# Performance work log

Hardware: AMD Instinct MI355X
Metric: run time of the kernel (lower is better)

## Reference

```python
import jax, jax.numpy as jnp
import numpy as np

B, T, F_IN, H = 64, 256, 2048, 1024


def setup_inputs() -> dict:
    key = jax.random.key(0)
    ks = jax.random.split(key, 8)
    s = 1.0 / np.sqrt(H)
    return {
        "input_var": jax.random.normal(ks[0], (B, T, F_IN), dtype=jnp.float32),
        "input_lengths": jax.random.randint(ks[1], (B,), 1, T + 1, dtype=jnp.int32),
        "W_p": jax.random.uniform(ks[2], (H, F_IN), jnp.float32, -s, s),
        "b_p": jax.random.uniform(ks[3], (H,), jnp.float32, -s, s),
        "w_ih": jax.random.uniform(ks[4], (3 * H, H), jnp.float32, -s, s),
        "w_hh": jax.random.uniform(ks[5], (3 * H, H), jnp.float32, -s, s),
        "b_ih": jax.random.uniform(ks[6], (3 * H,), jnp.float32, -s, s),
        "b_hh": jax.random.uniform(ks[7], (3 * H,), jnp.float32, -s, s),
    }


def reference(input_var, input_lengths, W_p, b_p, w_ih, w_hh, b_ih, b_hh):
    # project video features: (B,T,F) -> (B,T,H)
    emb = jnp.einsum("btf,hf->bth", input_var, W_p) + b_p
    # precompute input-gate contributions for all timesteps: (B,T,3H)
    gx = jnp.einsum("bth,gh->btg", emb, w_ih) + b_ih
    gx_t = jnp.swapaxes(gx, 0, 1)  # time-major (T,B,3H)
    t_idx = jnp.arange(T)
    mask_t = (t_idx[:, None] < input_lengths[None, :])  # (T,B)

    def step(h, inp):
        gi, m = inp  # gi: (B,3H), m: (B,)
        gh = h @ w_hh.T + b_hh  # (B,3H)
        r = jax.nn.sigmoid(gi[:, :H] + gh[:, :H])
        z = jax.nn.sigmoid(gi[:, H:2 * H] + gh[:, H:2 * H])
        n = jnp.tanh(gi[:, 2 * H:] + r * gh[:, 2 * H:])
        h_new = (1.0 - z) * n + z * h
        m2 = m[:, None]
        h = jnp.where(m2, h_new, h)           # packed: hidden frozen past length
        y = jnp.where(m2, h_new, 0.0)         # pad_packed: zeros past length
        return h, y

    h0 = jnp.zeros((B, H), dtype=input_var.dtype)
    _, ys = jax.lax.scan(step, h0, (gx_t, mask_t))  # ys: (T,B,H)
    output = jnp.swapaxes(ys, 0, 1)  # (B,T,H)
    hidden = output[:, -1, :]
    return (output, hidden)
```

## Files before the change

kernel.cpp:

```cpp
#include <hip/hip_runtime.h>
#include <stdint.h>


typedef __bf16 bfx8 __attribute__((ext_vector_type(8)));
typedef float  f32x4 __attribute__((ext_vector_type(4)));
typedef unsigned u32x4 __attribute__((ext_vector_type(4)));
typedef unsigned long long ull;

__global__ void cvt_bf16(const float* __restrict__ in, __bf16* __restrict__ out, int n8) {
    for (int i = blockIdx.x * blockDim.x + threadIdx.x; i < n8; i += gridDim.x * blockDim.x) {
        float4 a = ((const float4*)in)[2 * i];
        float4 b = ((const float4*)in)[2 * i + 1];
        union { __bf16 h[8]; uint4 v; } u;
        u.h[0] = (__bf16)a.x; u.h[1] = (__bf16)a.y; u.h[2] = (__bf16)a.z; u.h[3] = (__bf16)a.w;
        u.h[4] = (__bf16)b.x; u.h[5] = (__bf16)b.y; u.h[6] = (__bf16)b.z; u.h[7] = (__bf16)b.w;
        ((uint4*)out)[i] = u.v;
    }
}

__device__ __forceinline__ void g2l16(const void* g, void* l) {
    __builtin_amdgcn_global_load_lds(
        (__attribute__((address_space(1))) void*)g,
        (__attribute__((address_space(3))) void*)l,
        16, 0, 0);
}


__device__ __forceinline__ void stage_half16(const char* mat, int row0, size_t Kb, int tk,
                                             char* ldsHalf, int sr, int scb, int wave) {
    const char* s0 = mat + (size_t)(row0 + sr) * Kb + ((size_t)tk << 7) + scb;
    g2l16(s0, ldsHalf + (wave << 10));
    g2l16(s0 + (Kb << 6), ldsHalf + 8192 + (wave << 10));
}

#define MFMA16 __builtin_amdgcn_mfma_f32_16x16x32_bf16

template <bool OUTBF16>
__global__ __launch_bounds__(512)
void gemm256(const __bf16* __restrict__ A, const __bf16* __restrict__ W,
             const float* __restrict__ bias, void* __restrict__ C,
             int M, int N, int K)
{
    __shared__ char smem[131072];
    const int tid  = threadIdx.x;
    const int wave = tid >> 6, lane = tid & 63;
    const int q = lane >> 4, r15 = lane & 15;
    const int wm = wave >> 2, wn = wave & 3;

    const int nbx = N >> 8;
    const int nwg = (M >> 8) * nbx;
    const int cpx = nwg >> 3;
    const int wg  = (blockIdx.x & 7) * cpx + (blockIdx.x >> 3);
    const int m0  = (wg / nbx) << 8, n0 = (wg % nbx) << 8;
    const size_t Kb = (size_t)K << 1;
    const int NT = K >> 6;

    const int sr  = tid >> 3;
    const int scb = ((tid ^ (tid >> 3)) & 7) << 4;
    const int sx  = r15 & 7;
    const int la0 = r15 * 128 + ((q ^ sx) << 4);
    const int la1 = r15 * 128 + (((q | 4) ^ sx) << 4);

    const char* Ac = (const char*)A;
    const char* Wc = (const char*)W;

#pragma unroll
    for (int t = 0; t < 2; ++t) {
        char* ab = smem + (t << 15);
        char* bb = smem + 65536 + (t << 15);
        stage_half16(Ac, m0,       Kb, t, ab,         sr, scb, wave);
        stage_half16(Ac, m0 + 128, Kb, t, ab + 16384, sr, scb, wave);
        stage_half16(Wc, n0,       Kb, t, bb,         sr, scb, wave);
        stage_half16(Wc, n0 + 128, Kb, t, bb + 16384, sr, scb, wave);
    }
    asm volatile("s_waitcnt vmcnt(8)" ::: "memory");
    __builtin_amdgcn_s_barrier();

    f32x4 acc[8][4] = {};

    for (int t = 0; t < NT; ++t) {
        const int bsel = t & 1;
        const char* Ab = smem + (bsel << 15) + (wm << 14);
        const char* Bb = smem + 65536 + (bsel << 15) + ((wn >> 1) << 14) + ((wn & 1) << 13);
        const int t2 = t + 2;
        const bool st = t2 < NT;

        bfx8 aw[4][2], b01[2][2], b23[2][2];

#pragma unroll
        for (int m = 0; m < 4; ++m) {
            aw[m][0] = *(const bfx8*)(Ab + (m << 11) + la0);
            aw[m][1] = *(const bfx8*)(Ab + (m << 11) + la1);
        }
#pragma unroll
        for (int n = 0; n < 2; ++n) {
            b01[n][0] = *(const bfx8*)(Bb + (n << 11) + la0);
            b01[n][1] = *(const bfx8*)(Bb + (n << 11) + la1);
        }
        __builtin_amdgcn_s_barrier();
        asm volatile("s_waitcnt lgkmcnt(0)" ::: "memory");
        __builtin_amdgcn_s_setprio(1);
#pragma unroll
        for (int m = 0; m < 4; ++m)
#pragma unroll
            for (int n = 0; n < 2; ++n) {
                acc[m][n] = MFMA16(aw[m][0], b01[n][0], acc[m][n], 0, 0, 0);
                acc[m][n] = MFMA16(aw[m][1], b01[n][1], acc[m][n], 0, 0, 0);
            }
        __builtin_amdgcn_s_setprio(0);
        __builtin_amdgcn_s_barrier();

#pragma unroll
        for (int n = 0; n < 2; ++n) {
            b23[n][0] = *(const bfx8*)(Bb + ((n + 2) << 11) + la0);
            b23[n][1] = *(const bfx8*)(Bb + ((n + 2) << 11) + la1);
        }
        if (st) {
            char* bb = smem + 65536 + (bsel << 15);
            stage_half16(Wc, n0,       Kb, t2, bb,         sr, scb, wave);
            stage_half16(Wc, n0 + 128, Kb, t2, bb + 16384, sr, scb, wave);
        }
        __builtin_amdgcn_s_barrier();
        asm volatile("s_waitcnt lgkmcnt(0)" ::: "memory");
        __builtin_amdgcn_s_setprio(1);
#pragma unroll
        for (int m = 0; m < 4; ++m)
#pragma unroll
            for (int n = 0; n < 2; ++n) {
                acc[m][n + 2] = MFMA16(aw[m][0], b23[n][0], acc[m][n + 2], 0, 0, 0);
                acc[m][n + 2] = MFMA16(aw[m][1], b23[n][1], acc[m][n + 2], 0, 0, 0);
            }
        __builtin_amdgcn_s_setprio(0);
        __builtin_amdgcn_s_barrier();

#pragma unroll
        for (int m = 0; m < 4; ++m) {
            aw[m][0] = *(const bfx8*)(Ab + 8192 + (m << 11) + la0);
            aw[m][1] = *(const bfx8*)(Ab + 8192 + (m << 11) + la1);
        }
        if (st) {
            char* ab = smem + (bsel << 15);
            stage_half16(Ac, m0,       Kb, t2, ab,         sr, scb, wave);
            stage_half16(Ac, m0 + 128, Kb, t2, ab + 16384, sr, scb, wave);
        }
        __builtin_amdgcn_s_barrier();
        asm volatile("s_waitcnt lgkmcnt(0)" ::: "memory");
        __builtin_amdgcn_s_setprio(1);
#pragma unroll
        for (int m = 0; m < 4; ++m)
#pragma unroll
            for (int n = 0; n < 2; ++n) {
                acc[m + 4][n + 2] = MFMA16(aw[m][0], b23[n][0], acc[m + 4][n + 2], 0, 0, 0);
                acc[m + 4][n + 2] = MFMA16(aw[m][1], b23[n][1], acc[m + 4][n + 2], 0, 0, 0);
            }
        __builtin_amdgcn_s_setprio(0);
        __builtin_amdgcn_s_barrier();

        if (t < NT - 2) asm volatile("s_waitcnt vmcnt(8)" ::: "memory");
        else            asm volatile("s_waitcnt vmcnt(0)" ::: "memory");
        __builtin_amdgcn_s_barrier();
        __builtin_amdgcn_s_setprio(1);
#pragma unroll
        for (int m = 0; m < 4; ++m)
#pragma unroll
            for (int n = 0; n < 2; ++n) {
                acc[m + 4][n] = MFMA16(aw[m][0], b01[n][0], acc[m + 4][n], 0, 0, 0);
                acc[m + 4][n] = MFMA16(aw[m][1], b01[n][1], acc[m + 4][n], 0, 0, 0);
            }
        __builtin_amdgcn_s_setprio(0);
        __builtin_amdgcn_s_barrier();
    }

#pragma unroll
    for (int nf = 0; nf < 4; ++nf) {
        const int col = n0 + (wn << 6) + (nf << 4) + r15;
        const float bv = bias[col];
#pragma unroll
        for (int mf = 0; mf < 8; ++mf) {
#pragma unroll
            for (int i = 0; i < 4; ++i) {
                const int row = m0 + (wm << 7) + (mf << 4) + (q << 2) + i;
                const float v = acc[mf][nf][i] + bv;
                if (OUTBF16) ((__bf16*)C)[(size_t)row * N + col] = (__bf16)v;
                else         ((float*)C)[(size_t)row * N + col]  = v;
            }
        }
    }
}

__device__ __forceinline__ float sigm(float x) { return 1.f / (1.f + __expf(-x)); }
__device__ __forceinline__ float tanh_f(float x) { float e = __expf(2.f * x); return 1.f - 2.f / (e + 1.f); }

#define RP 1032

__global__ __launch_bounds__(256, 1)
void rnn_kernel(const float* __restrict__ gx, const int* __restrict__ lens,
                const __bf16* __restrict__ whhb, const float* __restrict__ b_hh,
                char* __restrict__ hbuf,
                float* __restrict__ out,
                unsigned* __restrict__ flags)
{
    __shared__ __bf16 hs[16 * RP];
    __shared__ float  ghs2[3 * 4 * 256];

    const int tid  = threadIdx.x;
    const int wave = tid >> 6, lane = tid & 63;
    const int q = lane >> 4, r15 = lane & 15;
    const int bb = (blockIdx.x & 7) >> 1;
    const int bj = ((blockIdx.x >> 3) << 1) | (blockIdx.x & 1);

    bfx8 Bf[3][8];
#pragma unroll
    for (int g = 0; g < 3; ++g)
#pragma unroll
        for (int kk = 0; kk < 8; ++kk)
            Bf[g][kk] = *(const bfx8*)(whhb
                + ((size_t)((g << 10) + (bj << 4) + r15) << 10)
                + (wave << 8) + (kk << 5) + (q << 3));

    const int m_ = tid >> 4, jj_ = tid & 15;
    const int bglob = (bb << 4) + m_;
    const int jglob = (bj << 4) + jj_;
    const float bhr = b_hh[jglob], bhz = b_hh[1024 + jglob], bhn = b_hh[2048 + jglob];
    const int mylen = lens[bglob];
    const int pd   = (tid & 127) >> 1;
    const int pblk = ((pd >> 1) << 3) | (bb << 1) | (pd & 1);
    const unsigned* fpoll = &flags[pblk << 4];

    const float* gp = gx + (size_t)bglob * 256 * 3072 + jglob;
    float gir = gp[0], giz = gp[1024], gin = gp[2048];
    float hstate = 0.f;

    for (int t = 0; t < 256; ++t) {
        if (t > 0) {
            unsigned tgt = (unsigned)t;
            while (__hip_atomic_load(fpoll, __ATOMIC_RELAXED, __HIP_MEMORY_SCOPE_AGENT) < tgt)
                __builtin_amdgcn_s_sleep(1);
            asm volatile("" ::: "memory");
        }
        {
            const char* sb = hbuf + ((t & 1) << 17) + (bb << 15) + (tid << 4);
            u32x4 r0, r1, r2, r3, r4, r5, r6, r7;
            asm volatile(
                "global_load_dwordx4 %0, %8, off sc1\n\t"
                "global_load_dwordx4 %1, %9, off sc1\n\t"
                "global_load_dwordx4 %2, %10, off sc1\n\t"
                "global_load_dwordx4 %3, %11, off sc1\n\t"
                "global_load_dwordx4 %4, %12, off sc1\n\t"
                "global_load_dwordx4 %5, %13, off sc1\n\t"
                "global_load_dwordx4 %6, %14, off sc1\n\t"
                "global_load_dwordx4 %7, %15, off sc1\n\t"
                "s_waitcnt vmcnt(0)"
                : "=&v"(r0), "=&v"(r1), "=&v"(r2), "=&v"(r3),
                  "=&v"(r4), "=&v"(r5), "=&v"(r6), "=&v"(r7)
                : "v"(sb),          "v"(sb + 4096),  "v"(sb + 8192),  "v"(sb + 12288),
                  "v"(sb + 16384),  "v"(sb + 20480), "v"(sb + 24576), "v"(sb + 28672)
                : "memory");
            const int colb = (tid & 127) << 4;
            const int mh = tid >> 7;
            char* hsb = (char*)hs;
            *(u32x4*)(hsb + (2 * 0 + mh) * 2064 + colb) = r0;
            *(u32x4*)(hsb + (2 * 1 + mh) * 2064 + colb) = r1;
            *(u32x4*)(hsb + (2 * 2 + mh) * 2064 + colb) = r2;
            *(u32x4*)(hsb + (2 * 3 + mh) * 2064 + colb) = r3;
            *(u32x4*)(hsb + (2 * 4 + mh) * 2064 + colb) = r4;
            *(u32x4*)(hsb + (2 * 5 + mh) * 2064 + colb) = r5;
            *(u32x4*)(hsb + (2 * 6 + mh) * 2064 + colb) = r6;
            *(u32x4*)(hsb + (2 * 7 + mh) * 2064 + colb) = r7;
        }
        __syncthreads();

        {
            f32x4 a0 = {0.f, 0.f, 0.f, 0.f}, a1 = a0, a2 = a0;
            const __bf16* hrow = &hs[r15 * RP + (wave << 8)];
#pragma unroll
            for (int kk = 0; kk < 8; ++kk) {
                bfx8 a = *(const bfx8*)(hrow + (kk << 5) + (q << 3));
                a0 = __builtin_amdgcn_mfma_f32_16x16x32_bf16(a, Bf[0][kk], a0, 0, 0, 0);
                a1 = __builtin_amdgcn_mfma_f32_16x16x32_bf16(a, Bf[1][kk], a1, 0, 0, 0);
                a2 = __builtin_amdgcn_mfma_f32_16x16x32_bf16(a, Bf[2][kk], a2, 0, 0, 0);
            }
#pragma unroll
            for (int i2 = 0; i2 < 4; ++i2) {
                int di = (((q << 2) + i2) << 4) + r15;
                ghs2[(wave << 8) + di]        = a0[i2];
                ghs2[1024 + (wave << 8) + di] = a1[i2];
                ghs2[2048 + (wave << 8) + di] = a2[i2];
            }
        }
        __syncthreads();

        float ghr = ghs2[tid] + ghs2[256 + tid] + ghs2[512 + tid] + ghs2[768 + tid] + bhr;
        float ghz = ghs2[1024 + tid] + ghs2[1280 + tid] + ghs2[1536 + tid] + ghs2[1792 + tid] + bhz;
        float ghn = ghs2[2048 + tid] + ghs2[2304 + tid] + ghs2[2560 + tid] + ghs2[2816 + tid] + bhn;
        float rg = sigm(gir + ghr);
        float zg = sigm(giz + ghz);
        float ng = tanh_f(gin + rg * ghn);
        float hnew = (1.f - zg) * ng + zg * hstate;
        bool mk = t < mylen;
        hstate = mk ? hnew : hstate;
        float y = mk ? hnew : 0.f;

        if (t < 255) {
            union { unsigned short us; __bf16 h; } cv; cv.h = (__bf16)hstate;
            unsigned hb = cv.us;
            unsigned nb = (unsigned)__shfl_xor((int)hb, 1);
            if (!(tid & 1)) {
                unsigned dv = hb | (nb << 16);
                unsigned* hw = (unsigned*)(hbuf + (((t + 1) & 1) << 17)
                             + (bglob << 11) + ((bj << 4) + jj_) * 2);
                __hip_atomic_store(hw, dv, __ATOMIC_RELAXED, __HIP_MEMORY_SCOPE_AGENT);
            }
            __syncthreads();
            if (tid == 0)
                __hip_atomic_store(&flags[blockIdx.x << 4], (unsigned)(t + 1),
                                   __ATOMIC_RELAXED, __HIP_MEMORY_SCOPE_AGENT);
            out[(size_t)(bglob * 256 + t) * 1024 + jglob] = y;
            gp += 3072;
            gir = gp[0]; giz = gp[1024]; gin = gp[2048];
        } else {
            out[(size_t)(bglob * 256 + t) * 1024 + jglob] = y;
            out[(size_t)(64 * 256) * 1024 + ((size_t)bglob << 10) + jglob] = y;
        }
    }
}

extern "C" void kernel_launch(void* const* d_in, const int* in_sizes, int n_in,
                              void* d_out, int out_size, void* d_ws, size_t ws_size,
                              hipStream_t stream) {
    const float* input = (const float*)d_in[0];
    const int*   lens  = (const int*)d_in[1];
    const float* W_p   = (const float*)d_in[2];
    const float* b_p   = (const float*)d_in[3];
    const float* w_ih  = (const float*)d_in[4];
    const float* w_hh  = (const float*)d_in[5];
    const float* b_ih  = (const float*)d_in[6];
    const float* b_hh  = (const float*)d_in[7];
    float* out = (float*)d_out;
    char* ws = (char*)d_ws;

    __bf16* Xb   = (__bf16*)(ws + 0);
    __bf16* Wpb  = (__bf16*)(ws + 67108864);
    __bf16* wihb = (__bf16*)(ws + 71303168);
    __bf16* whhb = (__bf16*)(ws + 77594624);
    __bf16* embb = (__bf16*)(ws + 83886080);
    float*  gx   = (float*) (ws + 117440512);
    char* hbuf   = ws + 318767104;
    unsigned* flags = (unsigned*)(ws + 319029248);

    hipMemsetAsync(ws + 318767104, 0, 262144 + 16384, stream);

    cvt_bf16<<<4096, 256, 0, stream>>>(input, Xb, 33554432 / 8);
    cvt_bf16<<<1024, 256, 0, stream>>>(W_p,  Wpb, 2097152 / 8);
    cvt_bf16<<<1536, 256, 0, stream>>>(w_ih, wihb, 3145728 / 8);
    cvt_bf16<<<1536, 256, 0, stream>>>(w_hh, whhb, 3145728 / 8);

    gemm256<true><<<dim3(256), 512, 0, stream>>>(Xb, Wpb, b_p, embb, 16384, 1024, 2048);
    gemm256<false><<<dim3(768), 512, 0, stream>>>(embb, wihb, b_ih, gx, 16384, 3072, 1024);

    rnn_kernel<<<256, 256, 0, stream>>>(gx, lens, whhb, b_hh, hbuf, out, flags);
}
```

Measured before the change: 978.4 us.

## Fuse input-gate projection into recurrent kernel, removing the gx GEMM

Drops the separate emb×w_ih GEMM and its large fp32 gx intermediate. Each RNN block now keeps its w_ih slice in registers and computes the input-gate contributions for step t+1 with MFMA while waiting on step t. The bf16 embedding rows are double-buffered through LDS and prefetched two steps ahead. This removes a full GEMM launch and the gx write/read traffic, but adds register pressure (a second 48-fragment weight set), extra LDS, and more MFMA work inside the latency-critical serial loop.

```diff
diff --git a/kernel.cpp b/kernel.cpp
--- a/kernel.cpp
+++ b/kernel.cpp
@@ -25,6 +25,7 @@
         16, 0, 0);
 }
 
+#define MFMA16 __builtin_amdgcn_mfma_f32_16x16x32_bf16
 
 __device__ __forceinline__ void stage_half16(const char* mat, int row0, size_t Kb, int tk,
                                              char* ldsHalf, int sr, int scb, int wave) {
@@ -32,8 +33,6 @@
     g2l16(s0, ldsHalf + (wave << 10));
     g2l16(s0 + (Kb << 6), ldsHalf + 8192 + (wave << 10));
 }
-
-#define MFMA16 __builtin_amdgcn_mfma_f32_16x16x32_bf16
 
 template <bool OUTBF16>
 __global__ __launch_bounds__(512)
@@ -194,14 +193,16 @@
 #define RP 1032
 
 __global__ __launch_bounds__(256, 1)
-void rnn_kernel(const float* __restrict__ gx, const int* __restrict__ lens,
-                const __bf16* __restrict__ whhb, const float* __restrict__ b_hh,
+void rnn_kernel(const __bf16* __restrict__ emb, const int* __restrict__ lens,
+                const __bf16* __restrict__ whhb, const __bf16* __restrict__ wihb,
+                const float* __restrict__ b_hh, const float* __restrict__ b_ih,
                 char* __restrict__ hbuf,
                 float* __restrict__ out,
                 unsigned* __restrict__ flags)
 {
     __shared__ __bf16 hs[16 * RP];
-    __shared__ float  ghs2[3 * 4 * 256];
+    __shared__ __bf16 ebs[2][16 * RP];
+    __shared__ float  ghs2[4 * 1024];
 
     const int tid  = threadIdx.x;
     const int wave = tid >> 6, lane = tid & 63;
@@ -209,29 +210,73 @@
     const int bb = (blockIdx.x & 7) >> 1;
     const int bj = ((blockIdx.x >> 3) << 1) | (blockIdx.x & 1);
 
-    bfx8 Bf[3][8];
+    bfx8 Bf[3][8], Wf[3][8];
 #pragma unroll
     for (int g = 0; g < 3; ++g)
 #pragma unroll
-        for (int kk = 0; kk < 8; ++kk)
-            Bf[g][kk] = *(const bfx8*)(whhb
-                + ((size_t)((g << 10) + (bj << 4) + r15) << 10)
-                + (wave << 8) + (kk << 5) + (q << 3));
+        for (int kk = 0; kk < 8; ++kk) {
+            const size_t ro = ((size_t)((g << 10) + (bj << 4) + r15) << 10)
+                            + (wave << 8) + (kk << 5) + (q << 3);
+            Bf[g][kk] = *(const bfx8*)(whhb + ro);
+            Wf[g][kk] = *(const bfx8*)(wihb + ro);
+        }
 
     const int m_ = tid >> 4, jj_ = tid & 15;
     const int bglob = (bb << 4) + m_;
     const int jglob = (bj << 4) + jj_;
-    const float bhr = b_hh[jglob], bhz = b_hh[1024 + jglob], bhn = b_hh[2048 + jglob];
+    const float br  = b_hh[jglob]        + b_ih[jglob];
+    const float bz  = b_hh[1024 + jglob] + b_ih[1024 + jglob];
+    const float bhn = b_hh[2048 + jglob];
+    const float bin = b_ih[2048 + jglob];
     const int mylen = lens[bglob];
     const int pd   = (tid & 127) >> 1;
     const int pblk = ((pd >> 1) << 3) | (bb << 1) | (pd & 1);
     const unsigned* fpoll = &flags[pblk << 4];
 
-    const float* gp = gx + (size_t)bglob * 256 * 3072 + jglob;
-    float gir = gp[0], giz = gp[1024], gin = gp[2048];
+    const int colb = (tid & 127) << 4;
+    const int mh   = tid >> 7;
+    const char* ebase = (const char*)emb + ((size_t)(bb << 4) * 256) * 2048;
+
     float hstate = 0.f;
+    const f32x4 z4 = {0.f, 0.f, 0.f, 0.f};
+    f32x4 giC0 = z4, giC1 = z4, giC2 = z4;
+
+    {
+        uint4 e0[8], e1[8];
+#pragma unroll
+        for (int rd = 0; rd < 8; ++rd) {
+            const char* s = ebase + (size_t)(2 * rd + mh) * 524288 + colb;
+            e0[rd] = *(const uint4*)(s);
+            e1[rd] = *(const uint4*)(s + 2048);
+        }
+        char* b0 = (char*)ebs[0]; char* b1 = (char*)ebs[1];
+#pragma unroll
+        for (int rd = 0; rd < 8; ++rd) {
+            *(uint4*)(b0 + (2 * rd + mh) * 2064 + colb) = e0[rd];
+            *(uint4*)(b1 + (2 * rd + mh) * 2064 + colb) = e1[rd];
+        }
+        __syncthreads();
+        const __bf16* er = &ebs[0][r15 * RP + (wave << 8)];
+#pragma unroll
+        for (int kk = 0; kk < 8; ++kk) {
+            bfx8 a = *(const bfx8*)(er + (kk << 5) + (q << 3));
+            giC0 = MFMA16(a, Wf[0][kk], giC0, 0, 0, 0);
+            giC1 = MFMA16(a, Wf[1][kk], giC1, 0, 0, 0);
+            giC2 = MFMA16(a, Wf[2][kk], giC2, 0, 0, 0);
+        }
+        __syncthreads();
+    }
 
     for (int t = 0; t < 256; ++t) {
+        uint4 e[8];
+        const bool stg = (t + 2) < 256;
+        if (stg) {
+            const char* s = ebase + (size_t)(t + 2) * 2048 + colb;
+#pragma unroll
+            for (int rd = 0; rd < 8; ++rd)
+                e[rd] = *(const uint4*)(s + (size_t)(2 * rd + mh) * 524288);
+        }
+
         if (t > 0) {
             unsigned tgt = (unsigned)t;
             while (__hip_atomic_load(fpoll, __ATOMIC_RELAXED, __HIP_MEMORY_SCOPE_AGENT) < tgt)
@@ -256,8 +301,6 @@
                 : "v"(sb),          "v"(sb + 4096),  "v"(sb + 8192),  "v"(sb + 12288),
                   "v"(sb + 16384),  "v"(sb + 20480), "v"(sb + 24576), "v"(sb + 28672)
                 : "memory");
-            const int colb = (tid & 127) << 4;
-            const int mh = tid >> 7;
             char* hsb = (char*)hs;
             *(u32x4*)(hsb + (2 * 0 + mh) * 2064 + colb) = r0;
             *(u32x4*)(hsb + (2 * 1 + mh) * 2064 + colb) = r1;
@@ -268,17 +311,23 @@
             *(u32x4*)(hsb + (2 * 6 + mh) * 2064 + colb) = r6;
             *(u32x4*)(hsb + (2 * 7 + mh) * 2064 + colb) = r7;
         }
+        if (stg) {
+            char* eb = (char*)ebs[t & 1];
+#pragma unroll
+            for (int rd = 0; rd < 8; ++rd)
+                *(uint4*)(eb + (2 * rd + mh) * 2064 + colb) = e[rd];
+        }
         __syncthreads();
 
         {
-            f32x4 a0 = {0.f, 0.f, 0.f, 0.f}, a1 = a0, a2 = a0;
+            f32x4 a0 = giC0, a1 = giC1, a2 = z4;
             const __bf16* hrow = &hs[r15 * RP + (wave << 8)];
 #pragma unroll
             for (int kk = 0; kk < 8; ++kk) {
                 bfx8 a = *(const bfx8*)(hrow + (kk << 5) + (q << 3));
-                a0 = __builtin_amdgcn_mfma_f32_16x16x32_bf16(a, Bf[0][kk], a0, 0, 0, 0);
-                a1 = __builtin_amdgcn_mfma_f32_16x16x32_bf16(a, Bf[1][kk], a1, 0, 0, 0);
-                a2 = __builtin_amdgcn_mfma_f32_16x16x32_bf16(a, Bf[2][kk], a2, 0, 0, 0);
+                a0 = MFMA16(a, Bf[0][kk], a0, 0, 0, 0);
+                a1 = MFMA16(a, Bf[1][kk], a1, 0, 0, 0);
+                a2 = MFMA16(a, Bf[2][kk], a2, 0, 0, 0);
             }
 #pragma unroll
             for (int i2 = 0; i2 < 4; ++i2) {
@@ -286,20 +335,35 @@
                 ghs2[(wave << 8) + di]        = a0[i2];
                 ghs2[1024 + (wave << 8) + di] = a1[i2];
                 ghs2[2048 + (wave << 8) + di] = a2[i2];
+                ghs2[3072 + (wave << 8) + di] = giC2[i2];
+            }
+        }
+
+        f32x4 g0 = z4, g1 = z4, g2 = z4;
+        if (t < 255) {
+            const __bf16* er = &ebs[(t + 1) & 1][r15 * RP + (wave << 8)];
+#pragma unroll
+            for (int kk = 0; kk < 8; ++kk) {
+                bfx8 a = *(const bfx8*)(er + (kk << 5) + (q << 3));
+                g0 = MFMA16(a, Wf[0][kk], g0, 0, 0, 0);
+                g1 = MFMA16(a, Wf[1][kk], g1, 0, 0, 0);
+                g2 = MFMA16(a, Wf[2][kk], g2, 0, 0, 0);
             }
         }
         __syncthreads();
 
-        float ghr = ghs2[tid] + ghs2[256 + tid] + ghs2[512 + tid] + ghs2[768 + tid] + bhr;
-        float ghz = ghs2[1024 + tid] + ghs2[1280 + tid] + ghs2[1536 + tid] + ghs2[1792 + tid] + bhz;
+        float rr  = ghs2[tid]        + ghs2[256 + tid]  + ghs2[512 + tid]  + ghs2[768 + tid]  + br;
+        float zz  = ghs2[1024 + tid] + ghs2[1280 + tid] + ghs2[1536 + tid] + ghs2[1792 + tid] + bz;
         float ghn = ghs2[2048 + tid] + ghs2[2304 + tid] + ghs2[2560 + tid] + ghs2[2816 + tid] + bhn;
-        float rg = sigm(gir + ghr);
-        float zg = sigm(giz + ghz);
+        float gin = ghs2[3072 + tid] + ghs2[3328 + tid] + ghs2[3584 + tid] + ghs2[3840 + tid] + bin;
+        float rg = sigm(rr);
+        float zg = sigm(zz);
         float ng = tanh_f(gin + rg * ghn);
         float hnew = (1.f - zg) * ng + zg * hstate;
         bool mk = t < mylen;
         hstate = mk ? hnew : hstate;
         float y = mk ? hnew : 0.f;
+        giC0 = g0; giC1 = g1; giC2 = g2;
 
         if (t < 255) {
             union { unsigned short us; __bf16 h; } cv; cv.h = (__bf16)hstate;
@@ -316,8 +380,6 @@
                 __hip_atomic_store(&flags[blockIdx.x << 4], (unsigned)(t + 1),
                                    __ATOMIC_RELAXED, __HIP_MEMORY_SCOPE_AGENT);
             out[(size_t)(bglob * 256 + t) * 1024 + jglob] = y;
-            gp += 3072;
-            gir = gp[0]; giz = gp[1024]; gin = gp[2048];
         } else {
             out[(size_t)(bglob * 256 + t) * 1024 + jglob] = y;
             out[(size_t)(64 * 256) * 1024 + ((size_t)bglob << 10) + jglob] = y;
@@ -344,7 +406,6 @@
     __bf16* wihb = (__bf16*)(ws + 71303168);
     __bf16* whhb = (__bf16*)(ws + 77594624);
     __bf16* embb = (__bf16*)(ws + 83886080);
-    float*  gx   = (float*) (ws + 117440512);
     char* hbuf   = ws + 318767104;
     unsigned* flags = (unsigned*)(ws + 319029248);
 
@@ -356,7 +417,7 @@
     cvt_bf16<<<1536, 256, 0, stream>>>(w_hh, whhb, 3145728 / 8);
 
     gemm256<true><<<dim3(256), 512, 0, stream>>>(Xb, Wpb, b_p, embb, 16384, 1024, 2048);
-    gemm256<false><<<dim3(768), 512, 0, stream>>>(embb, wihb, b_ih, gx, 16384, 3072, 1024);
-
-    rnn_kernel<<<256, 256, 0, stream>>>(gx, lens, whhb, b_hh, hbuf, out, flags);
-}
+
+    rnn_kernel<<<256, 256, 0, stream>>>(embb, lens, whhb, wihb, b_hh, b_ih,
+                                        hbuf, out, flags);
+}
```

Result: slower. 1.479 ms (+51.1%).
